# Kernel tuning notes

Hardware: AMD Instinct MI355X
Metric: run time of the kernel (lower is better)

Reference implementation:

```python
import jax, jax.numpy as jnp
import numpy as np

B, S, F, H, P = 256, 336, 8, 512, 96


def _lstm_step(h, c, x, Wih, Whh, b):
    # PyTorch gate order: input, forget, cell(g), output
    gates = x @ Wih.T + h @ Whh.T + b  # [B, 4H]
    i, f, g, o = jnp.split(gates, 4, axis=-1)
    c_new = jax.nn.sigmoid(f) * c + jax.nn.sigmoid(i) * jnp.tanh(g)
    h_new = jax.nn.sigmoid(o) * jnp.tanh(c_new)
    return h_new, c_new


def setup_inputs() -> dict:
    key = jax.random.key(0)
    ks = jax.random.split(key, 9)
    s_enc = 1.0 / np.sqrt(H)
    return {
        "x_enc": jax.random.normal(ks[0], (B, S, F), jnp.float32),
        "enc_Wih": jax.random.uniform(ks[1], (4 * H, F), jnp.float32, -s_enc, s_enc),
        "enc_Whh": jax.random.uniform(ks[2], (4 * H, H), jnp.float32, -s_enc, s_enc),
        "enc_b": jax.random.uniform(ks[3], (4 * H,), jnp.float32, -s_enc, s_enc),
        "dec_Wih": jax.random.uniform(ks[4], (4 * H, 1), jnp.float32, -s_enc, s_enc),
        "dec_Whh": jax.random.uniform(ks[5], (4 * H, H), jnp.float32, -s_enc, s_enc),
        "dec_b": jax.random.uniform(ks[6], (4 * H,), jnp.float32, -s_enc, s_enc),
        "lin_W": jax.random.uniform(ks[7], (1, H), jnp.float32, -s_enc, s_enc),
        "lin_b": jax.random.uniform(ks[8], (1,), jnp.float32, -s_enc, s_enc),
    }


def reference(x_enc, enc_Wih, enc_Whh, enc_b, dec_Wih, dec_Whh, dec_b, lin_W, lin_b):
    # ---- Encoder: single-layer LSTM over the sequence; keep final (h, c) ----
    def enc_step(carry, x_t):
        h, c = carry
        h, c = _lstm_step(h, c, x_t, enc_Wih, enc_Whh, enc_b)
        return (h, c), None

    h0 = jnp.zeros((B, H), x_enc.dtype)
    c0 = jnp.zeros((B, H), x_enc.dtype)
    xs = jnp.transpose(x_enc, (1, 0, 2))  # [S, B, F]
    (h_enc, c_enc), _ = jax.lax.scan(enc_step, (h0, c0), xs)

    x_dec0 = x_enc[:, -1, 3:4]  # [B, 1] -- feature index 3 of last timestep

    def dec_step(carry, _):
        h, c, x = carry
        h, c = _lstm_step(h, c, x, dec_Wih, dec_Whh, dec_b)
        y = h @ lin_W.T + lin_b  # [B, 1]
        return (h, c, y), y

    _, ys = jax.lax.scan(dec_step, (h_enc, c_enc, x_dec0), None, length=P)
    # ys: [P, B, 1] -> [B, P, 1]
    return jnp.transpose(ys, (1, 0, 2))
```

## Files before the change

### kernel.cpp

```cpp
#include <hip/hip_runtime.h>


typedef _Float16 half8 __attribute__((ext_vector_type(8)));
typedef float f32x4 __attribute__((ext_vector_type(4)));
typedef unsigned long long ull;

#define B_SZ 256
#define S_LEN 336
#define P_LEN 96
#define H_SZ 512
#define T_TOT (S_LEN + P_LEN)

#define SZ_PACK (16*8*17*64*8*2)
#define OFF_PACK 0
#define OFF_HBUF (3*SZ_PACK)
#define SZ_HBUF (2*B_SZ*H_SZ*2)
#define OFF_YBUF (OFF_HBUF + SZ_HBUF)
#define SZ_YBUF (P_LEN*B_SZ*128*4)
#define OFF_FLG (OFF_YBUF + SZ_YBUF)
#define SZ_FLG (16*16*4)

__device__ __forceinline__ float sigf(float x){
  return __builtin_amdgcn_rcpf(1.f + __expf(-x));
}
__device__ __forceinline__ float tanh_fast(float x){
  return 2.f*__builtin_amdgcn_rcpf(1.f + __expf(-2.f*x)) - 1.f;
}

__global__ void pack_weights(const float* __restrict__ Whh,
                             const float* __restrict__ Wih,
                             const float* __restrict__ linW,
                             _Float16* __restrict__ dst, int mode){
  int lane = threadIdx.x;
  int s = blockIdx.x, w = blockIdx.y, og = blockIdx.z;
  int col16 = lane & 15, hi = lane >> 4;
  int gatei = col16 >> 2, uloc = col16 & 3;
  int grow = gatei*H_SZ + og*32 + w*4 + uloc;
  half8 v;
  #pragma unroll
  for (int j = 0; j < 8; j++){
    int k = s*32 + hi*8 + j;
    float x = 0.f;
    if (k < H_SZ){
      x = Whh[(size_t)grow*H_SZ + k];
      if (mode == 2) x += Wih[grow]*linW[k];
    } else if (mode == 0 && k < H_SZ + 8){
      x = Wih[(size_t)grow*8 + (k - H_SZ)];
    } else if (mode == 1 && k == H_SZ){
      x = Wih[grow];
    }
    v[j] = (_Float16)x;
  }
  *(half8*)(dst + ((size_t)(((og*8 + w)*17 + s)*64 + lane))*8) = v;
}

__global__ void finalize_out(const float* __restrict__ y_buf,
                             const float* __restrict__ lin_b,
                             float* __restrict__ out){
  int i = blockIdx.x*256 + threadIdx.x;
  int b = i / P_LEN, td = i % P_LEN;
  const float* p = y_buf + ((size_t)td*B_SZ + b)*128;
  float s = lin_b[0];
  #pragma unroll
  for (int q = 0; q < 128; q++) s += p[q];
  out[i] = s;
}

__global__ __launch_bounds__(512) void lstm_main(
    const float* __restrict__ x_enc, const float* __restrict__ enc_b,
    const float* __restrict__ dec_b, const float* __restrict__ dec_Wih,
    const float* __restrict__ lin_W, const float* __restrict__ lin_b,
    const _Float16* __restrict__ pack,
    ull* __restrict__ h_buf,
    float* __restrict__ y_buf,
    unsigned int* __restrict__ blkflags)
{
  const int bx = blockIdx.x;
  const int og = bx >> 4, bg = bx & 15;
  const int tid = threadIdx.x;
  const int w = tid >> 6, lane = tid & 63;
  const int col16 = lane & 15, hi = lane >> 4;
  const int gatei = col16 >> 2;
  const int q4 = col16 & 3;
  const int unit = og*32 + w*4 + q4;
  const int grow = gatei*H_SZ + unit;
  const int r0 = bg*16;

  __shared__ __align__(16) unsigned char Abuf[16*1152];
  __shared__ unsigned lds_arrive;

  if (tid == 0) lds_arrive = 0;

  const _Float16* packBase = pack + ((size_t)((og*8 + w)*17)*64 + lane)*8;
  const size_t setStride = (size_t)SZ_PACK/2;

  half8 Breg[17];
  #pragma unroll
  for (int s = 0; s < 17; s++)
    Breg[s] = *(const half8*)(packBase + (size_t)s*64*8);

  const float encb = enc_b[grow];
  const float decb = dec_b[grow];
  const float wihg = dec_Wih[grow];
  const float linw = lin_W[unit];
  const float lbv  = lin_b[0];
  float bias = encb;
  float c4[4] = {0.f, 0.f, 0.f, 0.f};

  const int srow = tid >> 5, sseg = tid & 31;
  const int ssw  = (srow & 7) << 4;
  const int abase = col16*1152;
  const int asw   = (col16 & 7) << 4;

  for (int t = 0; t < T_TOT; t++){
    if (t == S_LEN){
      #pragma unroll
      for (int s = 0; s < 17; s++)
        Breg[s] = *(const half8*)(packBase + setStride + (size_t)s*64*8);
      bias = decb;
    } else if (t == S_LEN + 1){
      #pragma unroll
      for (int s = 0; s < 17; s++)
        Breg[s] = *(const half8*)(packBase + 2*setStride + (size_t)s*64*8);
      bias = decb + wihg*lbv;
    }

    float xv = 0.f;
    if (t < S_LEN){
      if (tid < 128)
        xv = x_enc[(size_t)(r0 + (tid >> 3))*(S_LEN*8) + t*8 + (tid & 7)];
    } else if (t == S_LEN){
      if (tid < 16)
        xv = x_enc[(size_t)(r0 + tid)*(S_LEN*8) + 335*8 + 3];
    }

    if (t > 0 && w == 0){
      const unsigned tgt = (unsigned)t;
      for(;;){
        unsigned f = tgt;
        if (lane < 16)
          f = __hip_atomic_load(&blkflags[bg*16 + lane], __ATOMIC_RELAXED,
                                __HIP_MEMORY_SCOPE_AGENT);
        if (__all(f >= tgt)) break;
      }
    }
    __syncthreads();

    if (t > 0){
      const ull* hs = h_buf + ((size_t)(((t-1)&1)*B_SZ + r0 + srow))*128 + sseg*4;
      ull d0 = __hip_atomic_load(hs+0, __ATOMIC_RELAXED, __HIP_MEMORY_SCOPE_AGENT);
      ull d1 = __hip_atomic_load(hs+1, __ATOMIC_RELAXED, __HIP_MEMORY_SCOPE_AGENT);
      ull d2 = __hip_atomic_load(hs+2, __ATOMIC_RELAXED, __HIP_MEMORY_SCOPE_AGENT);
      ull d3 = __hip_atomic_load(hs+3, __ATOMIC_RELAXED, __HIP_MEMORY_SCOPE_AGENT);
      uint4 A;  A.x = (unsigned)d0; A.y = (unsigned)(d0>>32);
                A.z = (unsigned)d1; A.w = (unsigned)(d1>>32);
      uint4 Bv; Bv.x = (unsigned)d2; Bv.y = (unsigned)(d2>>32);
                Bv.z = (unsigned)d3; Bv.w = (unsigned)(d3>>32);
      *(uint4*)&Abuf[srow*1152 + ((sseg*32     ) ^ ssw)] = A;
      *(uint4*)&Abuf[srow*1152 + ((sseg*32 + 16) ^ ssw)] = Bv;
    }
    if (t < S_LEN){
      if (tid < 128){
        int r = tid >> 3, f = tid & 7;
        *(_Float16*)&Abuf[r*1152 + (1024 ^ ((r & 7) << 4)) + f*2] = (_Float16)xv;
      }
      if (t == 0 && tid >= 256 && tid < 304){
        int idx = tid - 256;
        int r = idx & 15, u = 1 + (idx >> 4);
        uint4 z = {0, 0, 0, 0};
        *(uint4*)&Abuf[r*1152 + ((1024 + u*16) ^ ((r & 7) << 4))] = z;
      }
    } else if (t == S_LEN){
      if (tid < 16){
        half8 va;
        #pragma unroll
        for (int q = 0; q < 8; q++) va[q] = (_Float16)0.f;
        va[0] = (_Float16)xv;
        *(half8*)&Abuf[tid*1152 + (1024 ^ ((tid & 7) << 4))] = va;
      }
    }
    __syncthreads();

    f32x4 acc = {bias, bias, bias, bias};
    if (t == 0){
      half8 a = *(const half8*)&Abuf[abase + ((1024 + hi*16) ^ asw)];
      acc = __builtin_amdgcn_mfma_f32_16x16x32_f16(a, Breg[16], acc, 0, 0, 0);
    } else {
      f32x4 acc1 = {0.f, 0.f, 0.f, 0.f};
      #pragma unroll
      for (int s = 0; s < 16; s += 2){
        half8 a0 = *(const half8*)&Abuf[abase + (((s  )*64 + hi*16) ^ asw)];
        half8 a1 = *(const half8*)&Abuf[abase + (((s+1)*64 + hi*16) ^ asw)];
        acc  = __builtin_amdgcn_mfma_f32_16x16x32_f16(a0, Breg[s],   acc,  0, 0, 0);
        acc1 = __builtin_amdgcn_mfma_f32_16x16x32_f16(a1, Breg[s+1], acc1, 0, 0, 0);
      }
      if (t <= S_LEN){
        half8 a16 = *(const half8*)&Abuf[abase + ((16*64 + hi*16) ^ asw)];
        acc = __builtin_amdgcn_mfma_f32_16x16x32_f16(a16, Breg[16], acc, 0, 0, 0);
      }
      acc = acc + acc1;
    }

    float hold[4];
    #pragma unroll
    for (int j = 0; j < 4; j++){
      float a   = acc[j];
      float x4  = __shfl_xor(a, 4);
      float x8  = __shfl_xor(a, 8);
      float x12 = __shfl_xor(x4, 8);
      float gi, gf, gg, go;
      if      (gatei == 0){ gi = a;   gf = x4;  gg = x8;  go = x12; }
      else if (gatei == 1){ gi = x4;  gf = a;   gg = x12; go = x8;  }
      else if (gatei == 2){ gi = x8;  gf = x12; gg = a;   go = x4;  }
      else                { gi = x12; gf = x8;  gg = x4;  go = a;   }
      float cn = sigf(gf)*c4[j] + sigf(gi)*tanh_fast(gg);
      c4[j] = cn;
      hold[j] = sigf(go)*tanh_fast(cn);
    }

    unsigned short s16[4];
    #pragma unroll
    for (int j = 0; j < 4; j++)
      s16[j] = __builtin_bit_cast(unsigned short, (_Float16)hold[j]);
    unsigned lo01 = (unsigned)s16[0] | ((unsigned)s16[1] << 16);
    unsigned hi23 = (unsigned)s16[2] | ((unsigned)s16[3] << 16);
    const bool qlow = (q4 < 2), up = (q4 & 1);
    unsigned sendA = qlow ? hi23 : lo01;
    unsigned rA    = (unsigned)__shfl_xor((int)sendA, 2);
    unsigned keepA = qlow ? lo01 : hi23;
    unsigned vq_p  = up ? (keepA & 0xffffu) : (keepA >> 16);
    unsigned vqx_p = up ? (rA    & 0xffffu) : (rA    >> 16);
    unsigned sendB = qlow ? (vq_p | (vqx_p << 16)) : (vqx_p | (vq_p << 16));
    unsigned rB    = (unsigned)__shfl_xor((int)sendB, 1);
    unsigned vq_m  = up ? (keepA >> 16) : (keepA & 0xffffu);
    unsigned vqx_m = up ? (rA    >> 16) : (rA    & 0xffffu);
    unsigned ownB  = qlow ? (vq_m | (vqx_m << 16)) : (vqx_m | (vq_m << 16));
    unsigned w0 = up ? ((rB & 0xffffu) | (ownB << 16)) : ((ownB & 0xffffu) | (rB << 16));
    unsigned w1 = up ? ((rB >> 16) | (ownB & 0xffff0000u))
                     : ((ownB >> 16) | (rB & 0xffff0000u));
    if (gatei == 0){
      ull hv = (ull)w0 | ((ull)w1 << 32);
      int row = hi*4 + q4;
      __hip_atomic_store(h_buf + ((size_t)((t&1)*B_SZ + r0 + row))*128 + og*8 + w,
                         hv, __ATOMIC_RELAXED, __HIP_MEMORY_SCOPE_AGENT);
    }

    asm volatile("s_waitcnt vmcnt(0)" ::: "memory");
    if (lane == 0){
      unsigned old = atomicAdd(&lds_arrive, 1u);
      if (old == (unsigned)(t*8 + 7))
        __hip_atomic_store(&blkflags[bg*16 + og], (unsigned)(t + 1),
                           __ATOMIC_RELAXED, __HIP_MEMORY_SCOPE_AGENT);
    }

    if (t >= S_LEN){
      #pragma unroll
      for (int j = 0; j < 4; j++){
        float pv = (gatei == 0) ? hold[j]*linw : 0.f;
        pv += __shfl_xor(pv, 1);
        pv += __shfl_xor(pv, 2);
        if (col16 == 0)
          __hip_atomic_store(
              &y_buf[((size_t)(t - S_LEN)*B_SZ + r0 + hi*4 + j)*128 + og*8 + w],
              pv, __ATOMIC_RELAXED, __HIP_MEMORY_SCOPE_AGENT);
      }
    }
  }
}

extern "C" void kernel_launch(void* const* d_in, const int* in_sizes, int n_in,
                              void* d_out, int out_size, void* d_ws, size_t ws_size,
                              hipStream_t stream) {
  const float* x_enc   = (const float*)d_in[0];
  const float* enc_Wih = (const float*)d_in[1];
  const float* enc_Whh = (const float*)d_in[2];
  const float* enc_b   = (const float*)d_in[3];
  const float* dec_Wih = (const float*)d_in[4];
  const float* dec_Whh = (const float*)d_in[5];
  const float* dec_b   = (const float*)d_in[6];
  const float* lin_W   = (const float*)d_in[7];
  const float* lin_b   = (const float*)d_in[8];

  char* ws = (char*)d_ws;
  _Float16* pack  = (_Float16*)(ws + OFF_PACK);
  ull*      h_buf = (ull*)(ws + OFF_HBUF);
  float*    y_buf = (float*)(ws + OFF_YBUF);
  unsigned int* blkflags = (unsigned int*)(ws + OFF_FLG);

  hipMemsetAsync(ws + OFF_FLG, 0, SZ_FLG, stream);

  pack_weights<<<dim3(17, 8, 16), 64, 0, stream>>>(enc_Whh, enc_Wih, lin_W,
                                                   pack, 0);
  pack_weights<<<dim3(17, 8, 16), 64, 0, stream>>>(dec_Whh, dec_Wih, lin_W,
                                                   pack + SZ_PACK/2, 1);
  pack_weights<<<dim3(17, 8, 16), 64, 0, stream>>>(dec_Whh, dec_Wih, lin_W,
                                                   pack + SZ_PACK, 2);

  void* args[] = { (void*)&x_enc, (void*)&enc_b, (void*)&dec_b, (void*)&dec_Wih,
                   (void*)&lin_W, (void*)&lin_b, (void*)&pack,
                   (void*)&h_buf, (void*)&y_buf, (void*)&blkflags };
  hipLaunchCooperativeKernel((void*)lstm_main, dim3(256), dim3(512),
                             args, 0, stream);

  finalize_out<<<dim3((B_SZ*P_LEN)/256), 256, 0, stream>>>(y_buf, lin_b, (float*)d_out);
}
```

Baseline: 2.052 ms.

## Tag hidden-state words with step sequence numbers to poll data speculatively

Each 64-bit h_buf entry now holds 32 bits of fp16 hidden data plus the step number in the upper half. Blocks read their slice of h before waiting on the per-group flags, keep any words already tagged with the current step, and after the flag barrier re-poll only the stale ones. The aim is to overlap the global h loads with the flag spin and to drop the vmcnt(0) wait before the arrival counter. The cost is a doubled h buffer and its memset, twice as many stores and loads per step, and an extra __syncthreads after the MFMA loop.

Measured after the change: 4.332 ms. 111% more time.

```diff
diff --git a/kernel.cpp b/kernel.cpp
--- a/kernel.cpp
+++ b/kernel.cpp
@@ -14,11 +14,14 @@
 #define SZ_PACK (16*8*17*64*8*2)
 #define OFF_PACK 0
 #define OFF_HBUF (3*SZ_PACK)
-#define SZ_HBUF (2*B_SZ*H_SZ*2)
+#define SZ_HBUF (2*B_SZ*256*8)
 #define OFF_YBUF (OFF_HBUF + SZ_HBUF)
 #define SZ_YBUF (P_LEN*B_SZ*128*4)
 #define OFF_FLG (OFF_YBUF + SZ_YBUF)
 #define SZ_FLG (16*16*4)
+
+#define LDA(p) __hip_atomic_load((p), __ATOMIC_RELAXED, __HIP_MEMORY_SCOPE_AGENT)
+#define STA(p,v) __hip_atomic_store((p),(v), __ATOMIC_RELAXED, __HIP_MEMORY_SCOPE_AGENT)
 
 __device__ __forceinline__ float sigf(float x){
   return __builtin_amdgcn_rcpf(1.f + __expf(-x));
@@ -66,6 +69,16 @@
   out[i] = s;
 }
 
+#define VALBITS()                                    \
+    ((((unsigned)(v0 >> 32) != tgt) ? 1u   : 0u) |   \
+     (((unsigned)(v1 >> 32) != tgt) ? 2u   : 0u) |   \
+     (((unsigned)(v2 >> 32) != tgt) ? 4u   : 0u) |   \
+     (((unsigned)(v3 >> 32) != tgt) ? 8u   : 0u) |   \
+     (((unsigned)(v4 >> 32) != tgt) ? 16u  : 0u) |   \
+     (((unsigned)(v5 >> 32) != tgt) ? 32u  : 0u) |   \
+     (((unsigned)(v6 >> 32) != tgt) ? 64u  : 0u) |   \
+     (((unsigned)(v7 >> 32) != tgt) ? 128u : 0u))
+
 __global__ __launch_bounds__(512) void lstm_main(
     const float* __restrict__ x_enc, const float* __restrict__ enc_b,
     const float* __restrict__ dec_b, const float* __restrict__ dec_Wih,
@@ -88,7 +101,6 @@
 
   __shared__ __align__(16) unsigned char Abuf[16*1152];
   __shared__ unsigned lds_arrive;
-
   if (tid == 0) lds_arrive = 0;
 
   const _Float16* packBase = pack + ((size_t)((og*8 + w)*17)*64 + lane)*8;
@@ -134,31 +146,28 @@
         xv = x_enc[(size_t)(r0 + tid)*(S_LEN*8) + 335*8 + 3];
     }
 
-    if (t > 0 && w == 0){
-      const unsigned tgt = (unsigned)t;
-      for(;;){
-        unsigned f = tgt;
-        if (lane < 16)
-          f = __hip_atomic_load(&blkflags[bg*16 + lane], __ATOMIC_RELAXED,
-                                __HIP_MEMORY_SCOPE_AGENT);
-        if (__all(f >= tgt)) break;
-      }
-    }
-    __syncthreads();
-
+    const unsigned tgt = (unsigned)t;
+    const ull* base = h_buf
+        + ((size_t)(((t-1)&1)*B_SZ + r0 + srow))*256 + sseg*8;
+    ull v0=0, v1=0, v2=0, v3=0, v4=0, v5=0, v6=0, v7=0;
+    unsigned pend = 0, hadA = 0, hadB = 0;
     if (t > 0){
-      const ull* hs = h_buf + ((size_t)(((t-1)&1)*B_SZ + r0 + srow))*128 + sseg*4;
-      ull d0 = __hip_atomic_load(hs+0, __ATOMIC_RELAXED, __HIP_MEMORY_SCOPE_AGENT);
-      ull d1 = __hip_atomic_load(hs+1, __ATOMIC_RELAXED, __HIP_MEMORY_SCOPE_AGENT);
-      ull d2 = __hip_atomic_load(hs+2, __ATOMIC_RELAXED, __HIP_MEMORY_SCOPE_AGENT);
-      ull d3 = __hip_atomic_load(hs+3, __ATOMIC_RELAXED, __HIP_MEMORY_SCOPE_AGENT);
-      uint4 A;  A.x = (unsigned)d0; A.y = (unsigned)(d0>>32);
-                A.z = (unsigned)d1; A.w = (unsigned)(d1>>32);
-      uint4 Bv; Bv.x = (unsigned)d2; Bv.y = (unsigned)(d2>>32);
-                Bv.z = (unsigned)d3; Bv.w = (unsigned)(d3>>32);
-      *(uint4*)&Abuf[srow*1152 + ((sseg*32     ) ^ ssw)] = A;
-      *(uint4*)&Abuf[srow*1152 + ((sseg*32 + 16) ^ ssw)] = Bv;
-    }
+      v0 = LDA(base+0); v1 = LDA(base+1); v2 = LDA(base+2); v3 = LDA(base+3);
+      v4 = LDA(base+4); v5 = LDA(base+5); v6 = LDA(base+6); v7 = LDA(base+7);
+      pend = VALBITS();
+      hadA = pend & 0x0Fu; hadB = pend & 0xF0u;
+      if (!hadA){
+        uint4 A; A.x = (unsigned)v0; A.y = (unsigned)v1;
+                 A.z = (unsigned)v2; A.w = (unsigned)v3;
+        *(uint4*)&Abuf[srow*1152 + ((sseg*32) ^ ssw)] = A;
+      }
+      if (!hadB){
+        uint4 Bv; Bv.x = (unsigned)v4; Bv.y = (unsigned)v5;
+                  Bv.z = (unsigned)v6; Bv.w = (unsigned)v7;
+        *(uint4*)&Abuf[srow*1152 + ((sseg*32 + 16) ^ ssw)] = Bv;
+      }
+    }
+
     if (t < S_LEN){
       if (tid < 128){
         int r = tid >> 3, f = tid & 7;
@@ -174,9 +183,44 @@
       if (tid < 16){
         half8 va;
         #pragma unroll
-        for (int q = 0; q < 8; q++) va[q] = (_Float16)0.f;
+        for (int k = 0; k < 8; k++) va[k] = (_Float16)0.f;
         va[0] = (_Float16)xv;
         *(half8*)&Abuf[tid*1152 + (1024 ^ ((tid & 7) << 4))] = va;
+      }
+    }
+
+    if (t > 0 && w == 0){
+      for(;;){
+        unsigned f = tgt;
+        if (lane < 16)
+          f = LDA(&blkflags[bg*16 + lane]);
+        if (__all(f >= tgt)) break;
+      }
+    }
+    __syncthreads();
+
+    if (t > 0 && pend){
+      do {
+        if (pend & 1u)   v0 = LDA(base+0);
+        if (pend & 2u)   v1 = LDA(base+1);
+        if (pend & 4u)   v2 = LDA(base+2);
+        if (pend & 8u)   v3 = LDA(base+3);
+        if (pend & 16u)  v4 = LDA(base+4);
+        if (pend & 32u)  v5 = LDA(base+5);
+        if (pend & 64u)  v6 = LDA(base+6);
+        if (pend & 128u) v7 = LDA(base+7);
+        pend = VALBITS();
+        if (pend) __builtin_amdgcn_s_sleep(1);
+      } while (pend);
+      if (hadA){
+        uint4 A; A.x = (unsigned)v0; A.y = (unsigned)v1;
+                 A.z = (unsigned)v2; A.w = (unsigned)v3;
+        *(uint4*)&Abuf[srow*1152 + ((sseg*32) ^ ssw)] = A;
+      }
+      if (hadB){
+        uint4 Bv; Bv.x = (unsigned)v4; Bv.y = (unsigned)v5;
+                  Bv.z = (unsigned)v6; Bv.w = (unsigned)v7;
+        *(uint4*)&Abuf[srow*1152 + ((sseg*32 + 16) ^ ssw)] = Bv;
       }
     }
     __syncthreads();
@@ -200,6 +244,7 @@
       }
       acc = acc + acc1;
     }
+    __syncthreads();
 
     float hold[4];
     #pragma unroll
@@ -238,19 +283,19 @@
     unsigned w0 = up ? ((rB & 0xffffu) | (ownB << 16)) : ((ownB & 0xffffu) | (rB << 16));
     unsigned w1 = up ? ((rB >> 16) | (ownB & 0xffff0000u))
                      : ((ownB >> 16) | (rB & 0xffff0000u));
+
     if (gatei == 0){
-      ull hv = (ull)w0 | ((ull)w1 << 32);
       int row = hi*4 + q4;
-      __hip_atomic_store(h_buf + ((size_t)((t&1)*B_SZ + r0 + row))*128 + og*8 + w,
-                         hv, __ATOMIC_RELAXED, __HIP_MEMORY_SCOPE_AGENT);
-    }
-
-    asm volatile("s_waitcnt vmcnt(0)" ::: "memory");
+      ull* hb = h_buf + ((size_t)((t&1)*B_SZ + r0 + row))*256 + og*16 + w*2;
+      ull seqv = ((ull)(unsigned)(t + 1)) << 32;
+      STA(hb,     (ull)w0 | seqv);
+      STA(hb + 1, (ull)w1 | seqv);
+    }
+
     if (lane == 0){
       unsigned old = atomicAdd(&lds_arrive, 1u);
       if (old == (unsigned)(t*8 + 7))
-        __hip_atomic_store(&blkflags[bg*16 + og], (unsigned)(t + 1),
-                           __ATOMIC_RELAXED, __HIP_MEMORY_SCOPE_AGENT);
+        STA(&blkflags[bg*16 + og], (unsigned)(t + 1));
     }
 
     if (t >= S_LEN){
@@ -260,9 +305,8 @@
         pv += __shfl_xor(pv, 1);
         pv += __shfl_xor(pv, 2);
         if (col16 == 0)
-          __hip_atomic_store(
-              &y_buf[((size_t)(t - S_LEN)*B_SZ + r0 + hi*4 + j)*128 + og*8 + w],
-              pv, __ATOMIC_RELAXED, __HIP_MEMORY_SCOPE_AGENT);
+          STA(&y_buf[((size_t)(t - S_LEN)*B_SZ + r0 + hi*4 + j)*128 + og*8 + w],
+              pv);
       }
     }
   }
@@ -287,6 +331,7 @@
   float*    y_buf = (float*)(ws + OFF_YBUF);
   unsigned int* blkflags = (unsigned int*)(ws + OFF_FLG);
 
+  hipMemsetAsync(ws + OFF_HBUF, 0, SZ_HBUF, stream);
   hipMemsetAsync(ws + OFF_FLG, 0, SZ_FLG, stream);
 
   pack_weights<<<dim3(17, 8, 16), 64, 0, stream>>>(enc_Whh, enc_Wih, lin_W,
```
